# Kernel optimization log

Hardware: AMD Instinct MI355X
Metric: run time of the kernel (lower is better)

## Reference

```python
import jax, jax.numpy as jnp
import numpy as np

NH, HD = 8, 32  # num_heads, head_dim (fusion_dim=256)
BN_EPS = 1e-5

def conv1x1(x, W, b):
    # x: (B,Cin,H,W), W: (Cout,Cin), b: (Cout,)
    return jnp.einsum('oc,bchw->bohw', W, x) + b[None, :, None, None]

def mha(Q, K, V):
    # Q,K,V: (B,C,H,W); split channels into NH contiguous head chunks
    B, C, H, W = Q.shape
    N = H * W
    q = Q.reshape(B, NH, HD, N).transpose(0, 1, 3, 2)  # (B,nh,N,hd)
    k = K.reshape(B, NH, HD, N).transpose(0, 1, 3, 2)
    v = V.reshape(B, NH, HD, N).transpose(0, 1, 3, 2)
    scores = jnp.einsum('bhnd,bhmd->bhnm', q, k) / jnp.sqrt(jnp.float32(HD))
    attn = jax.nn.softmax(scores, axis=-1)  # dropout is identity in eval
    out = jnp.einsum('bhnm,bhmd->bhnd', attn, v)
    return out.transpose(0, 1, 3, 2).reshape(B, C, H, W)

def attention_map(Q, K, H, W):
    B, C = Q.shape[:2]
    N = H * W
    Qg = Q.reshape(B, NH, HD, N).mean(axis=-1)  # (B,nh,hd)
    Kg = K.reshape(B, NH, HD, N).mean(axis=-1)
    att = (Qg * Kg).sum(axis=-1).mean(axis=-1)  # (B,)
    return jnp.broadcast_to(att[:, None, None], (B, H, W))

def setup_inputs() -> dict:
    key = jax.random.key(0)
    ks = jax.random.split(key, 20)
    D = 256
    def w(k, o, i):
        return jax.random.normal(k, (o, i), dtype=jnp.float32) * 0.02
    def b(k, o):
        return jax.random.normal(k, (o,), dtype=jnp.float32) * 0.02
    return {
        'rgb_features': jax.random.normal(ks[0], (2, D, 56, 56), dtype=jnp.float32),
        'depth_features': jax.random.normal(ks[1], (2, D, 56, 56), dtype=jnp.float32),
        'Wq_rd': w(ks[2], D, D), 'bq_rd': b(ks[3], D),
        'Wk_d': w(ks[4], D, D), 'bk_d': b(ks[5], D),
        'Wv_d': w(ks[6], D, D), 'bv_d': b(ks[7], D),
        'Wq_dr': w(ks[8], D, D), 'bq_dr': b(ks[9], D),
        'Wk_r': w(ks[10], D, D), 'bk_r': b(ks[11], D),
        'Wv_r': w(ks[12], D, D), 'bv_r': b(ks[13], D),
        'Wf1': w(ks[14], D, 2 * D), 'bf1': b(ks[15], D),
        'gamma': jnp.ones((D,), jnp.float32), 'beta': jnp.zeros((D,), jnp.float32),
        'Wf2': w(ks[16], D, D), 'bf2': b(ks[17], D),
    }

def reference(rgb_features, depth_features, Wq_rd, bq_rd, Wk_d, bk_d, Wv_d, bv_d,
              Wq_dr, bq_dr, Wk_r, bk_r, Wv_r, bv_r, Wf1, bf1, gamma, beta, Wf2, bf2):
    B, _, H, W = rgb_features.shape
    Q_rgb = conv1x1(rgb_features, Wq_rd, bq_rd)
    K_depth = conv1x1(depth_features, Wk_d, bk_d)
    V_depth = conv1x1(depth_features, Wv_d, bv_d)
    rgb_attended = mha(Q_rgb, K_depth, V_depth)
    Q_depth = conv1x1(depth_features, Wq_dr, bq_dr)
    K_rgb = conv1x1(rgb_features, Wk_r, bk_r)
    V_rgb = conv1x1(rgb_features, Wv_r, bv_r)
    depth_attended = mha(Q_depth, K_rgb, V_rgb)
    fused = jnp.concatenate([rgb_attended, depth_attended], axis=1)
    h = conv1x1(fused, Wf1, bf1)
    # BatchNorm2d in eval mode: running_mean=0, running_var=1
    h = h / jnp.sqrt(jnp.float32(1.0 + BN_EPS)) * gamma[None, :, None, None] + beta[None, :, None, None]
    h = jax.nn.relu(h)
    fused_features = conv1x1(h, Wf2, bf2)
    amap = attention_map(Q_rgb, K_depth, H, W)
    return fused_features, amap
```

## Files before the change

### kernel.cpp

```cpp
#include <hip/hip_runtime.h>

typedef unsigned short u16;
typedef short bf8 __attribute__((ext_vector_type(8)));
typedef float f4 __attribute__((ext_vector_type(4)));
typedef unsigned short us4 __attribute__((ext_vector_type(4)));

#define DEV static __device__ __forceinline__

DEV u16 f2bf(float x) {
  union { float f; unsigned u; } v; v.f = x;
  unsigned r = v.u + 0x7fffu + ((v.u >> 16) & 1u);
  return (u16)(r >> 16);
}
DEV float bf2f(u16 h) {
  union { unsigned u; float f; } v; v.u = ((unsigned)h) << 16;
  return v.f;
}

constexpr int  NSP = 3136;
constexpr long SZ1 = 2l * 256 * NSP;
constexpr float SCQ = 0.2550205145980166f;
constexpr long OFF_XB  = 0;
constexpr long OFF_QB  = 2 * SZ1;
constexpr long OFF_KB  = 4 * SZ1;
constexpr long OFF_VB  = 6 * SZ1;
constexpr long OFF_ATT = 8 * SZ1;
constexpr long OFF_H   = 10 * SZ1;
constexpr long OFF_WC  = 11 * SZ1;
constexpr long OFF_WF1 = OFF_WC + 2l * 768 * 256;
constexpr long OFF_WF2 = OFF_WF1 + 256l * 512;
constexpr long END_BF16 = OFF_WF2 + 256l * 256;

__global__ __launch_bounds__(256) void k_cvt_x(const float* __restrict__ rgb,
                                               const float* __restrict__ dep,
                                               u16* __restrict__ xb) {
  __shared__ u16 xs[256][68];
  const int z = blockIdx.y;
  const int mod = z >> 1, b = z & 1;
  const float* s = (mod ? dep : rgb) + (long)b * 256 * NSP;
  const int n0 = blockIdx.x * 64;
  const int tid = threadIdx.x;
#pragma unroll
  for (int p = 0; p < 8; ++p) {
    const int c = p * 32 + (tid >> 3);
    const int nl = (tid & 7) * 8;
    f4 v0 = *(const f4*)(s + (long)c * NSP + n0 + nl);
    f4 v1 = *(const f4*)(s + (long)c * NSP + n0 + nl + 4);
    us4 o0, o1;
    o0.x = f2bf(v0.x); o0.y = f2bf(v0.y); o0.z = f2bf(v0.z); o0.w = f2bf(v0.w);
    o1.x = f2bf(v1.x); o1.y = f2bf(v1.y); o1.z = f2bf(v1.z); o1.w = f2bf(v1.w);
    *(us4*)(&xs[c][nl]) = o0;
    *(us4*)(&xs[c][nl + 4]) = o1;
  }
  __syncthreads();
  const int lane = tid & 63, ul = tid >> 6;
  const int g = lane >> 4, r = lane & 15;
  u16* dst = xb + (long)mod * SZ1 + (long)b * 802816
           + (((long)((n0 >> 4) + ul)) * 8) * 512 + lane * 8;
  const int nn = ul * 16 + r;
#pragma unroll
  for (int kblk = 0; kblk < 8; ++kblk) {
    const int c0 = kblk * 32 + g * 8;
    us4 lo, hi;
    lo.x = xs[c0 + 0][nn]; lo.y = xs[c0 + 1][nn]; lo.z = xs[c0 + 2][nn]; lo.w = xs[c0 + 3][nn];
    hi.x = xs[c0 + 4][nn]; hi.y = xs[c0 + 5][nn]; hi.z = xs[c0 + 6][nn]; hi.w = xs[c0 + 7][nn];
    *(us4*)(dst + kblk * 512) = lo;
    *(us4*)(dst + kblk * 512 + 4) = hi;
  }
}

__global__ __launch_bounds__(256) void k_prep(
    const float* __restrict__ wq_rd, const float* __restrict__ wk_r, const float* __restrict__ wv_r,
    const float* __restrict__ wq_dr, const float* __restrict__ wk_d, const float* __restrict__ wv_d,
    const float* __restrict__ wf1, const float* __restrict__ wf2,
    const float* __restrict__ bq_rd, const float* __restrict__ bk_r, const float* __restrict__ bv_r,
    const float* __restrict__ bq_dr, const float* __restrict__ bk_d, const float* __restrict__ bv_d,
    u16* __restrict__ wsb, float* __restrict__ bcat) {
  long idx = (long)blockIdx.x * 256 + threadIdx.x;
  const long WCN = 2l * 768 * 256;
  if (idx < WCN) {
    int mod = idx >= 768l * 256;
    long f = idx - (mod ? 768l * 256 : 0);
    int j = (int)f & 7, ln = ((int)f >> 3) & 63, unit = (int)(f >> 9);
    int kblk = unit & 7, mblk = unit >> 3;
    int row = mblk * 16 + (ln & 15), col = kblk * 32 + (ln >> 4) * 8 + j;
    int seg = row >> 8, r2 = row & 255;
    const float* src;
    if (!mod) src = seg == 0 ? wq_rd : (seg == 1 ? wk_r : wv_r);
    else      src = seg == 0 ? wq_dr : (seg == 1 ? wk_d : wv_d);
    wsb[OFF_WC + idx] = f2bf(src[r2 * 256 + col]);
    return;
  }
  long jx = idx - WCN;
  if (jx < 256l * 512) {
    int j = (int)jx & 7, ln = ((int)jx >> 3) & 63, unit = (int)(jx >> 9);
    int kblk = unit & 15, mblk = unit >> 4;
    int row = mblk * 16 + (ln & 15), col = kblk * 32 + (ln >> 4) * 8 + j;
    wsb[OFF_WF1 + jx] = f2bf(wf1[row * 512 + col]);
    return;
  }
  jx -= 256l * 512;
  if (jx < 256l * 256) {
    int j = (int)jx & 7, ln = ((int)jx >> 3) & 63, unit = (int)(jx >> 9);
    int kblk = unit & 7, mblk = unit >> 3;
    int row = mblk * 16 + (ln & 15), col = kblk * 32 + (ln >> 4) * 8 + j;
    wsb[OFF_WF2 + jx] = f2bf(wf2[row * 256 + col]);
    return;
  }
  jx -= 256l * 256;
  if (jx < 1536) {
    int mod = jx >= 768;
    int row = (int)jx - (mod ? 768 : 0);
    int seg = row >> 8, r2 = row & 255;
    const float* src;
    if (!mod) src = seg == 0 ? bq_rd : (seg == 1 ? bk_r : bv_r);
    else      src = seg == 0 ? bq_dr : (seg == 1 ? bk_d : bv_d);
    bcat[jx] = src[r2];
  }
}

template <int KDIM, int EPI>
__global__ __launch_bounds__(256) void k_gemm(
    u16* __restrict__ wsb, const float* __restrict__ bcat,
    const float* __restrict__ bf1, const float* __restrict__ gamma,
    const float* __restrict__ beta, const float* __restrict__ bf2,
    float* __restrict__ outf) {
  constexpr int KB = KDIM / 32;
  const int tid = threadIdx.x;
  const int lane = tid & 63, wid = tid >> 6;
  const int g = lane >> 4, r = lane & 15;
  const int wm = wid >> 1, wn = wid & 1;
  const int n0 = blockIdx.x * 64;
  const int m0 = blockIdx.y * 128;
  const int z = blockIdx.z;

  int b = 0, mod = 0;
  const u16* In; const u16* W;
  if constexpr (EPI == 0) {
    mod = z & 1; b = z >> 1;
    In = wsb + OFF_XB + (long)mod * SZ1 + (long)b * 802816;
    W  = wsb + OFF_WC + (long)mod * 768 * 256;
  } else if constexpr (EPI == 1) {
    b = z;
    In = wsb + OFF_ATT + (long)b * NSP * 512;
    W  = wsb + OFF_WF1;
  } else {
    b = z;
    In = wsb + OFF_H + (long)b * 802816;
    W  = wsb + OFF_WF2;
  }

  const int M0 = m0 + wm * 64;
  const u16* Abase = W + ((long)(M0 >> 4) * KB) * 512 + lane * 8;
  const u16* Bbase = In + ((long)((n0 >> 4) + wn * 2) * KB) * 512 + lane * 8;

  const f4 zero4 = {0.f, 0.f, 0.f, 0.f};
  f4 acc[4][2];
#pragma unroll
  for (int i = 0; i < 4; ++i)
#pragma unroll
    for (int j = 0; j < 2; ++j) acc[i][j] = zero4;

#pragma unroll 8
  for (int kb = 0; kb < KB; ++kb) {
    bf8 aw[4], bx[2];
#pragma unroll
    for (int i = 0; i < 4; ++i)
      aw[i] = *(const bf8*)(Abase + ((long)i * KB + kb) * 512);
#pragma unroll
    for (int jn = 0; jn < 2; ++jn)
      bx[jn] = *(const bf8*)(Bbase + ((long)jn * KB + kb) * 512);
#pragma unroll
    for (int i = 0; i < 4; ++i)
#pragma unroll
      for (int jn = 0; jn < 2; ++jn)
        acc[i][jn] = __builtin_amdgcn_mfma_f32_16x16x32_bf16(aw[i], bx[jn], acc[i][jn], 0, 0, 0);
  }

  const int seg = M0 >> 8;
#pragma unroll
  for (int i = 0; i < 4; ++i) {
    const int orow = M0 + i * 16 + 4 * g;
#pragma unroll
    for (int jn = 0; jn < 2; ++jn) {
      const int n = n0 + wn * 32 + jn * 16 + r;
      f4 a = acc[i][jn];
      if constexpr (EPI == 0) {
        const int ol = orow & 255;
        const float* bs = bcat + mod * 768 + seg * 256 + ol;
        const float qs = (seg == 0) ? SCQ : 1.0f;
        float a0 = (a.x + bs[0]) * qs, a1 = (a.y + bs[1]) * qs;
        float a2 = (a.z + bs[2]) * qs, a3 = (a.w + bs[3]) * qs;
        if (seg == 0) {
          const int hh = ol >> 5, hd0 = ol & 31;
          us4 pk; pk.x = f2bf(a0); pk.y = f2bf(a1); pk.z = f2bf(a2); pk.w = f2bf(a3);
          *(us4*)(wsb + OFF_QB + mod * SZ1
                  + (((long)(b * 8 + hh) * 196 + (n >> 4)) << 9)
                  + ((hd0 >> 3) * 16 + (n & 15)) * 8 + (hd0 & 7)) = pk;
        } else if (seg == 1) {
          const int hh = ol >> 5, hd0 = ol & 31;
          const int t = n >> 5, rr = n & 31;
          const int half = (rr >> 2) & 1, rK = ((rr >> 3) << 2) | (rr & 3);
          us4 pk; pk.x = f2bf(a0); pk.y = f2bf(a1); pk.z = f2bf(a2); pk.w = f2bf(a3);
          *(us4*)(wsb + OFF_KB + mod * SZ1
                  + ((((long)(b * 8 + hh) * 98 + t) * 2 + half) << 9)
                  + ((hd0 >> 3) * 16 + rK) * 8 + (hd0 & 7)) = pk;
        } else {
          const int hh = ol >> 5, rem = ol & 31, halfc = rem >> 4, rv = rem & 15;
          const int t = n >> 5, gp = (n >> 3) & 3, j = n & 7;
          u16* dst = wsb + OFF_VB + mod * SZ1
                   + ((((long)(b * 8 + hh) * 98 + t) * 2 + halfc) << 9)
                   + (gp * 16 + rv) * 8 + j;
          dst[0] = f2bf(a0); dst[8] = f2bf(a1); dst[16] = f2bf(a2); dst[24] = f2bf(a3);
        }
      } else if constexpr (EPI == 1) {
        us4 pk;
#pragma unroll
        for (int q = 0; q < 4; ++q) {
          const int o = orow + q;
          float v = (a[q] + bf1[o]) * (gamma[o] * 0.9999950000374994f) + beta[o];
          pk[q] = f2bf(fmaxf(v, 0.f));
        }
        const int ch0 = orow;
        *(us4*)(wsb + OFF_H + ((((long)b * 196 + (n >> 4)) * 8 + (ch0 >> 5)) << 9)
                + (((ch0 >> 3) & 3) * 16 + (n & 15)) * 8 + (ch0 & 7)) = pk;
      } else {
#pragma unroll
        for (int q = 0; q < 4; ++q) {
          const int o = orow + q;
          outf[(long)(b * 256 + o) * NSP + n] = a[q] + bf2[o];
        }
      }
    }
  }
}

DEV bf8 pack_p(f4 s0, f4 s1) {
  union { unsigned u[4]; bf8 v; } p;
  float a0 = __builtin_amdgcn_exp2f(s0.x), a1 = __builtin_amdgcn_exp2f(s0.y);
  float a2 = __builtin_amdgcn_exp2f(s0.z), a3 = __builtin_amdgcn_exp2f(s0.w);
  float a4 = __builtin_amdgcn_exp2f(s1.x), a5 = __builtin_amdgcn_exp2f(s1.y);
  float a6 = __builtin_amdgcn_exp2f(s1.z), a7 = __builtin_amdgcn_exp2f(s1.w);
  asm("v_cvt_pk_bf16_f32 %0, %1, %2" : "=v"(p.u[0]) : "v"(a0), "v"(a1));
  asm("v_cvt_pk_bf16_f32 %0, %1, %2" : "=v"(p.u[1]) : "v"(a2), "v"(a3));
  asm("v_cvt_pk_bf16_f32 %0, %1, %2" : "=v"(p.u[2]) : "v"(a4), "v"(a5));
  asm("v_cvt_pk_bf16_f32 %0, %1, %2" : "=v"(p.u[3]) : "v"(a6), "v"(a7));
  return p.v;
}

__global__ __launch_bounds__(256) void k_attn(u16* __restrict__ wsb) {
  const int m = blockIdx.z;
  const int bh = blockIdx.y;
  const int b = bh >> 3, h = bh & 7;
  const int tid = threadIdx.x;
  const int lane = tid & 63, wid = tid >> 6;
  const int qh = wid & 1, kvh = wid >> 1;
  const int g = lane >> 4, r = lane & 15;
  const int q0 = blockIdx.x * 64 + qh * 32;

  const u16* QF = wsb + OFF_QB + (long)m * SZ1 + ((long)bh * 196) * 512;
  const u16* KF = wsb + OFF_KB + (long)(1 - m) * SZ1 + ((long)bh * 196) * 512;
  const u16* VF = wsb + OFF_VB + (long)(1 - m) * SZ1 + ((long)bh * 196) * 512;

  const bf8 qfA = *(const bf8*)(QF + ((long)(q0 >> 4) << 9) + lane * 8);
  const bf8 qfB = *(const bf8*)(QF + ((long)((q0 >> 4) + 1) << 9) + lane * 8);
  const int kv0 = kvh ? 1600 : 0;
  const int kvn = kvh ? 1536 : 1600;
  const u16* kp = KF + ((long)(kv0 >> 5) << 10) + lane * 8;
  const u16* vp = VF + ((long)(kv0 >> 5) << 10) + lane * 8;

  bf8 ones;
#pragma unroll
  for (int j = 0; j < 8; ++j) ones[j] = (short)0x3F80;

  const f4 zero4 = {0.f, 0.f, 0.f, 0.f};
  f4 oA0 = zero4, oA1 = zero4, oB0 = zero4, oB1 = zero4;
  f4 lA = zero4, lB = zero4;

  for (int kv = 0; kv < kvn; kv += 64) {
    const bf8 kf0 = *(const bf8*)(kp);
    const bf8 kf1 = *(const bf8*)(kp + 512);
    const bf8 kf2 = *(const bf8*)(kp + 1024);
    const bf8 kf3 = *(const bf8*)(kp + 1536);
    kp += 2048;
    const bf8 v0a = *(const bf8*)(vp);
    const bf8 v1a = *(const bf8*)(vp + 512);
    const bf8 v0b = *(const bf8*)(vp + 1024);
    const bf8 v1b = *(const bf8*)(vp + 1536);
    vp += 2048;

    {
      f4 s0 = __builtin_amdgcn_mfma_f32_16x16x32_bf16(kf0, qfA, zero4, 0, 0, 0);
      f4 s1 = __builtin_amdgcn_mfma_f32_16x16x32_bf16(kf1, qfA, zero4, 0, 0, 0);
      f4 s2 = __builtin_amdgcn_mfma_f32_16x16x32_bf16(kf2, qfA, zero4, 0, 0, 0);
      f4 s3 = __builtin_amdgcn_mfma_f32_16x16x32_bf16(kf3, qfA, zero4, 0, 0, 0);
      bf8 p0 = pack_p(s0, s1);
      bf8 p1 = pack_p(s2, s3);
      lA  = __builtin_amdgcn_mfma_f32_16x16x32_bf16(ones, p0, lA, 0, 0, 0);
      lA  = __builtin_amdgcn_mfma_f32_16x16x32_bf16(ones, p1, lA, 0, 0, 0);
      oA0 = __builtin_amdgcn_mfma_f32_16x16x32_bf16(v0a, p0, oA0, 0, 0, 0);
      oA0 = __builtin_amdgcn_mfma_f32_16x16x32_bf16(v0b, p1, oA0, 0, 0, 0);
      oA1 = __builtin_amdgcn_mfma_f32_16x16x32_bf16(v1a, p0, oA1, 0, 0, 0);
      oA1 = __builtin_amdgcn_mfma_f32_16x16x32_bf16(v1b, p1, oA1, 0, 0, 0);
    }
    {
      f4 s0 = __builtin_amdgcn_mfma_f32_16x16x32_bf16(kf0, qfB, zero4, 0, 0, 0);
      f4 s1 = __builtin_amdgcn_mfma_f32_16x16x32_bf16(kf1, qfB, zero4, 0, 0, 0);
      f4 s2 = __builtin_amdgcn_mfma_f32_16x16x32_bf16(kf2, qfB, zero4, 0, 0, 0);
      f4 s3 = __builtin_amdgcn_mfma_f32_16x16x32_bf16(kf3, qfB, zero4, 0, 0, 0);
      bf8 p0 = pack_p(s0, s1);
      bf8 p1 = pack_p(s2, s3);
      lB  = __builtin_amdgcn_mfma_f32_16x16x32_bf16(ones, p0, lB, 0, 0, 0);
      lB  = __builtin_amdgcn_mfma_f32_16x16x32_bf16(ones, p1, lB, 0, 0, 0);
      oB0 = __builtin_amdgcn_mfma_f32_16x16x32_bf16(v0a, p0, oB0, 0, 0, 0);
      oB0 = __builtin_amdgcn_mfma_f32_16x16x32_bf16(v0b, p1, oB0, 0, 0, 0);
      oB1 = __builtin_amdgcn_mfma_f32_16x16x32_bf16(v1a, p0, oB1, 0, 0, 0);
      oB1 = __builtin_amdgcn_mfma_f32_16x16x32_bf16(v1b, p1, oB1, 0, 0, 0);
    }
  }

  __shared__ f4 so[2][4][64];
  __shared__ float sl[2][2][64];
  if (kvh) {
    so[qh][0][lane] = oA0; so[qh][1][lane] = oA1;
    so[qh][2][lane] = oB0; so[qh][3][lane] = oB1;
    sl[qh][0][lane] = lA.x; sl[qh][1][lane] = lB.x;
  }
  __syncthreads();
  if (!kvh) {
    oA0 += so[qh][0][lane]; oA1 += so[qh][1][lane];
    oB0 += so[qh][2][lane]; oB1 += so[qh][3][lane];
    const float invA = 1.0f / (lA.x + sl[qh][0][lane]);
    const float invB = 1.0f / (lB.x + sl[qh][1][lane]);
    oA0 *= invA; oA1 *= invA; oB0 *= invB; oB1 *= invB;

    u16* ab = wsb + OFF_ATT + ((((long)b * 196 + (q0 >> 4)) * 16) + m * 8 + h) * 512;
    const int ld0 = ((g >> 1) * 16 + r) * 8 + 4 * (g & 1);
    us4 w0, w1, w2, w3;
#pragma unroll
    for (int q = 0; q < 4; ++q) {
      w0[q] = f2bf(oA0[q]); w1[q] = f2bf(oA1[q]);
      w2[q] = f2bf(oB0[q]); w3[q] = f2bf(oB1[q]);
    }
    *(us4*)(ab + ld0) = w0;
    *(us4*)(ab + ld0 + 256) = w1;
    *(us4*)(ab + 8192 + ld0) = w2;
    *(us4*)(ab + 8192 + ld0 + 256) = w3;
  }
}

__global__ __launch_bounds__(256) void k_amap_red(const u16* __restrict__ wsb,
                                                  float* __restrict__ qsums,
                                                  float* __restrict__ ksums) {
  const int split = blockIdx.x;
  const int bh = blockIdx.y;
  const int t = threadIdx.x;
  const int d = t & 31, ns = t >> 5;
  const u16* qb = wsb + OFF_QB + ((long)bh * 196) * 512 + ((d >> 3) * 16) * 8 + (d & 7);
  const u16* kb = wsb + OFF_KB + SZ1 + ((long)bh * 196) * 512 + ((d >> 3) * 16) * 8 + (d & 7);
  float qs = 0.f, ks = 0.f;
  for (int u = split * 28 + ns; u < split * 28 + 28; u += 8) {
    const long ub = (long)u << 9;
#pragma unroll
    for (int rr = 0; rr < 16; ++rr) {
      qs += bf2f(qb[ub + rr * 8]);
      ks += bf2f(kb[ub + rr * 8]);
    }
  }
  __shared__ float sq[256], sk[256];
  sq[t] = qs; sk[t] = ks;
  __syncthreads();
  if (t < 32) {
#pragma unroll
    for (int j = 1; j < 8; ++j) { qs += sq[t + 32 * j]; ks += sk[t + 32 * j]; }
    atomicAdd(qsums + bh * 32 + t, qs);
    atomicAdd(ksums + bh * 32 + t, ks);
  }
}

__global__ __launch_bounds__(256) void k_amap_fin(const float* __restrict__ qsums,
                                                  const float* __restrict__ ksums,
                                                  float* __restrict__ att2) {
  const int b = blockIdx.x, t = threadIdx.x;
  float v = qsums[b * 256 + t] * ksums[b * 256 + t];
  __shared__ float sd[256];
  sd[t] = v; __syncthreads();
#pragma unroll
  for (int off = 128; off; off >>= 1) {
    if (t < off) sd[t] += sd[t + off];
    __syncthreads();
  }
  if (t == 0) att2[b] = sd[0] * (1.0f / (8.0f * 3136.0f * 3136.0f * SCQ));
}

__global__ void k_amap_wr(const float* __restrict__ att2, float* __restrict__ outf) {
  const int b = blockIdx.y;
  const int i = blockIdx.x * 256 + threadIdx.x;
  if (i < NSP) outf[2l * 256 * NSP + (long)b * NSP + i] = att2[b];
}

extern "C" void kernel_launch(void* const* d_in, const int* in_sizes, int n_in,
                              void* d_out, int out_size, void* d_ws, size_t ws_size,
                              hipStream_t stream) {
  const float* rgb   = (const float*)d_in[0];
  const float* dep   = (const float*)d_in[1];
  const float* Wq_rd = (const float*)d_in[2];
  const float* bq_rd = (const float*)d_in[3];
  const float* Wk_d  = (const float*)d_in[4];
  const float* bk_d  = (const float*)d_in[5];
  const float* Wv_d  = (const float*)d_in[6];
  const float* bv_d  = (const float*)d_in[7];
  const float* Wq_dr = (const float*)d_in[8];
  const float* bq_dr = (const float*)d_in[9];
  const float* Wk_r  = (const float*)d_in[10];
  const float* bk_r  = (const float*)d_in[11];
  const float* Wv_r  = (const float*)d_in[12];
  const float* bv_r  = (const float*)d_in[13];
  const float* Wf1   = (const float*)d_in[14];
  const float* bf1   = (const float*)d_in[15];
  const float* gamma = (const float*)d_in[16];
  const float* beta  = (const float*)d_in[17];
  const float* Wf2   = (const float*)d_in[18];
  const float* bf2   = (const float*)d_in[19];
  float* out = (float*)d_out;

  u16* wsb = (u16*)d_ws;
  float* wsf = (float*)((char*)d_ws + (size_t)END_BF16 * 2);
  float* att2  = wsf;
  float* qsums = wsf + 4;
  float* ksums = wsf + 4 + 512;
  float* bcat  = wsf + 4 + 1024;
  const size_t needed = (size_t)END_BF16 * 2 + (4 + 1024 + 1536) * sizeof(float);
  if (ws_size < needed) return;

  hipMemsetAsync(wsf, 0, (4 + 1024) * sizeof(float), stream);
  k_cvt_x<<<dim3(49, 4), 256, 0, stream>>>(rgb, dep, wsb);
  k_prep<<<2310, 256, 0, stream>>>(Wq_rd, Wk_r, Wv_r, Wq_dr, Wk_d, Wv_d, Wf1, Wf2,
                                   bq_rd, bk_r, bv_r, bq_dr, bk_d, bv_d, wsb, bcat);
  k_gemm<256, 0><<<dim3(49, 6, 4), 256, 0, stream>>>(wsb, bcat, nullptr, nullptr, nullptr, nullptr, nullptr);
  k_attn<<<dim3(49, 16, 2), 256, 0, stream>>>(wsb);
  k_amap_red<<<dim3(7, 16), 256, 0, stream>>>(wsb, qsums, ksums);
  k_amap_fin<<<2, 256, 0, stream>>>(qsums, ksums, att2);
  k_amap_wr<<<dim3(13, 2), 256, 0, stream>>>(att2, out);
  k_gemm<512, 1><<<dim3(49, 2, 2), 256, 0, stream>>>(wsb, nullptr, bf1, gamma, beta, nullptr, nullptr);
  k_gemm<256, 2><<<dim3(49, 2, 2), 256, 0, stream>>>(wsb, nullptr, nullptr, nullptr, nullptr, bf2, out);
}
```

Before: 119.0 us.

## Give each attention wave all 64 queries and split keys four ways

Each wave now processes all 64 query rows of the block (four Q fragments) against a quarter of the key/value range, instead of two waves per query half each taking half of the keys. Every K/V fragment loaded from global memory is therefore reused across four query tiles rather than two, halving K/V load traffic per unit of MFMA work. The cost is more accumulator registers per wave (8 output f4s plus 4 row sums), a larger shared-memory reduction across three waves, and a longer serial epilogue in wave 0.

Result: no change. 119.8 us (+0.7%).

```diff
diff --git a/kernel.cpp b/kernel.cpp
--- a/kernel.cpp
+++ b/kernel.cpp
@@ -253,31 +253,34 @@
   const int bh = blockIdx.y;
   const int b = bh >> 3, h = bh & 7;
   const int tid = threadIdx.x;
-  const int lane = tid & 63, wid = tid >> 6;
-  const int qh = wid & 1, kvh = wid >> 1;
+  const int lane = tid & 63, kvh = tid >> 6;
   const int g = lane >> 4, r = lane & 15;
-  const int q0 = blockIdx.x * 64 + qh * 32;
+  const int q0 = blockIdx.x * 64;
 
   const u16* QF = wsb + OFF_QB + (long)m * SZ1 + ((long)bh * 196) * 512;
   const u16* KF = wsb + OFF_KB + (long)(1 - m) * SZ1 + ((long)bh * 196) * 512;
   const u16* VF = wsb + OFF_VB + (long)(1 - m) * SZ1 + ((long)bh * 196) * 512;
 
-  const bf8 qfA = *(const bf8*)(QF + ((long)(q0 >> 4) << 9) + lane * 8);
-  const bf8 qfB = *(const bf8*)(QF + ((long)((q0 >> 4) + 1) << 9) + lane * 8);
-  const int kv0 = kvh ? 1600 : 0;
-  const int kvn = kvh ? 1536 : 1600;
-  const u16* kp = KF + ((long)(kv0 >> 5) << 10) + lane * 8;
-  const u16* vp = VF + ((long)(kv0 >> 5) << 10) + lane * 8;
+  bf8 qf[4];
+#pragma unroll
+  for (int j = 0; j < 4; ++j)
+    qf[j] = *(const bf8*)(QF + ((long)((q0 >> 4) + j) << 9) + lane * 8);
+
+  const int tb = kvh ? (13 + 12 * (kvh - 1)) : 0;
+  const int te = tb + (kvh ? 12 : 13);
+  const u16* kp = KF + ((long)tb << 11) + lane * 8;
+  const u16* vp = VF + ((long)tb << 11) + lane * 8;
 
   bf8 ones;
 #pragma unroll
   for (int j = 0; j < 8; ++j) ones[j] = (short)0x3F80;
 
   const f4 zero4 = {0.f, 0.f, 0.f, 0.f};
-  f4 oA0 = zero4, oA1 = zero4, oB0 = zero4, oB1 = zero4;
-  f4 lA = zero4, lB = zero4;
-
-  for (int kv = 0; kv < kvn; kv += 64) {
+  f4 o[4][2], l[4];
+#pragma unroll
+  for (int j = 0; j < 4; ++j) { o[j][0] = zero4; o[j][1] = zero4; l[j] = zero4; }
+
+  for (int t = tb; t < te; ++t) {
     const bf8 kf0 = *(const bf8*)(kp);
     const bf8 kf1 = *(const bf8*)(kp + 512);
     const bf8 kf2 = *(const bf8*)(kp + 1024);
@@ -289,63 +292,71 @@
     const bf8 v1b = *(const bf8*)(vp + 1536);
     vp += 2048;
 
-    {
-      f4 s0 = __builtin_amdgcn_mfma_f32_16x16x32_bf16(kf0, qfA, zero4, 0, 0, 0);
-      f4 s1 = __builtin_amdgcn_mfma_f32_16x16x32_bf16(kf1, qfA, zero4, 0, 0, 0);
-      f4 s2 = __builtin_amdgcn_mfma_f32_16x16x32_bf16(kf2, qfA, zero4, 0, 0, 0);
-      f4 s3 = __builtin_amdgcn_mfma_f32_16x16x32_bf16(kf3, qfA, zero4, 0, 0, 0);
-      bf8 p0 = pack_p(s0, s1);
-      bf8 p1 = pack_p(s2, s3);
-      lA  = __builtin_amdgcn_mfma_f32_16x16x32_bf16(ones, p0, lA, 0, 0, 0);
-      lA  = __builtin_amdgcn_mfma_f32_16x16x32_bf16(ones, p1, lA, 0, 0, 0);
-      oA0 = __builtin_amdgcn_mfma_f32_16x16x32_bf16(v0a, p0, oA0, 0, 0, 0);
-      oA0 = __builtin_amdgcn_mfma_f32_16x16x32_bf16(v0b, p1, oA0, 0, 0, 0);
-      oA1 = __builtin_amdgcn_mfma_f32_16x16x32_bf16(v1a, p0, oA1, 0, 0, 0);
-      oA1 = __builtin_amdgcn_mfma_f32_16x16x32_bf16(v1b, p1, oA1, 0, 0, 0);
+#pragma unroll
+    for (int pr = 0; pr < 2; ++pr) {
+      const bf8 qA = qf[pr * 2], qB = qf[pr * 2 + 1];
+      f4 sA0 = __builtin_amdgcn_mfma_f32_16x16x32_bf16(kf0, qA, zero4, 0, 0, 0);
+      f4 sA1 = __builtin_amdgcn_mfma_f32_16x16x32_bf16(kf1, qA, zero4, 0, 0, 0);
+      f4 sA2 = __builtin_amdgcn_mfma_f32_16x16x32_bf16(kf2, qA, zero4, 0, 0, 0);
+      f4 sA3 = __builtin_amdgcn_mfma_f32_16x16x32_bf16(kf3, qA, zero4, 0, 0, 0);
+      f4 sB0 = __builtin_amdgcn_mfma_f32_16x16x32_bf16(kf0, qB, zero4, 0, 0, 0);
+      f4 sB1 = __builtin_amdgcn_mfma_f32_16x16x32_bf16(kf1, qB, zero4, 0, 0, 0);
+      f4 sB2 = __builtin_amdgcn_mfma_f32_16x16x32_bf16(kf2, qB, zero4, 0, 0, 0);
+      f4 sB3 = __builtin_amdgcn_mfma_f32_16x16x32_bf16(kf3, qB, zero4, 0, 0, 0);
+      bf8 pA0 = pack_p(sA0, sA1);
+      bf8 pA1 = pack_p(sA2, sA3);
+      bf8 pB0 = pack_p(sB0, sB1);
+      bf8 pB1 = pack_p(sB2, sB3);
+      const int jA = pr * 2, jB = pr * 2 + 1;
+      l[jA]    = __builtin_amdgcn_mfma_f32_16x16x32_bf16(ones, pA0, l[jA], 0, 0, 0);
+      l[jA]    = __builtin_amdgcn_mfma_f32_16x16x32_bf16(ones, pA1, l[jA], 0, 0, 0);
+      l[jB]    = __builtin_amdgcn_mfma_f32_16x16x32_bf16(ones, pB0, l[jB], 0, 0, 0);
+      l[jB]    = __builtin_amdgcn_mfma_f32_16x16x32_bf16(ones, pB1, l[jB], 0, 0, 0);
+      o[jA][0] = __builtin_amdgcn_mfma_f32_16x16x32_bf16(v0a, pA0, o[jA][0], 0, 0, 0);
+      o[jA][0] = __builtin_amdgcn_mfma_f32_16x16x32_bf16(v0b, pA1, o[jA][0], 0, 0, 0);
+      o[jA][1] = __builtin_amdgcn_mfma_f32_16x16x32_bf16(v1a, pA0, o[jA][1], 0, 0, 0);
+      o[jA][1] = __builtin_amdgcn_mfma_f32_16x16x32_bf16(v1b, pA1, o[jA][1], 0, 0, 0);
+      o[jB][0] = __builtin_amdgcn_mfma_f32_16x16x32_bf16(v0a, pB0, o[jB][0], 0, 0, 0);
+      o[jB][0] = __builtin_amdgcn_mfma_f32_16x16x32_bf16(v0b, pB1, o[jB][0], 0, 0, 0);
+      o[jB][1] = __builtin_amdgcn_mfma_f32_16x16x32_bf16(v1a, pB0, o[jB][1], 0, 0, 0);
+      o[jB][1] = __builtin_amdgcn_mfma_f32_16x16x32_bf16(v1b, pB1, o[jB][1], 0, 0, 0);
     }
-    {
-      f4 s0 = __builtin_amdgcn_mfma_f32_16x16x32_bf16(kf0, qfB, zero4, 0, 0, 0);
-      f4 s1 = __builtin_amdgcn_mfma_f32_16x16x32_bf16(kf1, qfB, zero4, 0, 0, 0);
-      f4 s2 = __builtin_amdgcn_mfma_f32_16x16x32_bf16(kf2, qfB, zero4, 0, 0, 0);
-      f4 s3 = __builtin_amdgcn_mfma_f32_16x16x32_bf16(kf3, qfB, zero4, 0, 0, 0);
-      bf8 p0 = pack_p(s0, s1);
-      bf8 p1 = pack_p(s2, s3);
-      lB  = __builtin_amdgcn_mfma_f32_16x16x32_bf16(ones, p0, lB, 0, 0, 0);
-      lB  = __builtin_amdgcn_mfma_f32_16x16x32_bf16(ones, p1, lB, 0, 0, 0);
-      oB0 = __builtin_amdgcn_mfma_f32_16x16x32_bf16(v0a, p0, oB0, 0, 0, 0);
-      oB0 = __builtin_amdgcn_mfma_f32_16x16x32_bf16(v0b, p1, oB0, 0, 0, 0);
-      oB1 = __builtin_amdgcn_mfma_f32_16x16x32_bf16(v1a, p0, oB1, 0, 0, 0);
-      oB1 = __builtin_amdgcn_mfma_f32_16x16x32_bf16(v1b, p1, oB1, 0, 0, 0);
+  }
+
+  __shared__ f4 so[3][8][64];
+  __shared__ float sl[3][4][64];
+  if (kvh) {
+#pragma unroll
+    for (int j = 0; j < 4; ++j) {
+      so[kvh - 1][j * 2][lane] = o[j][0];
+      so[kvh - 1][j * 2 + 1][lane] = o[j][1];
+      sl[kvh - 1][j][lane] = l[j].x;
     }
-  }
-
-  __shared__ f4 so[2][4][64];
-  __shared__ float sl[2][2][64];
-  if (kvh) {
-    so[qh][0][lane] = oA0; so[qh][1][lane] = oA1;
-    so[qh][2][lane] = oB0; so[qh][3][lane] = oB1;
-    sl[qh][0][lane] = lA.x; sl[qh][1][lane] = lB.x;
   }
   __syncthreads();
   if (!kvh) {
-    oA0 += so[qh][0][lane]; oA1 += so[qh][1][lane];
-    oB0 += so[qh][2][lane]; oB1 += so[qh][3][lane];
-    const float invA = 1.0f / (lA.x + sl[qh][0][lane]);
-    const float invB = 1.0f / (lB.x + sl[qh][1][lane]);
-    oA0 *= invA; oA1 *= invA; oB0 *= invB; oB1 *= invB;
-
+#pragma unroll
+    for (int w = 0; w < 3; ++w)
+#pragma unroll
+      for (int j = 0; j < 4; ++j) {
+        o[j][0] += so[w][j * 2][lane];
+        o[j][1] += so[w][j * 2 + 1][lane];
+        l[j].x += sl[w][j][lane];
+      }
     u16* ab = wsb + OFF_ATT + ((((long)b * 196 + (q0 >> 4)) * 16) + m * 8 + h) * 512;
     const int ld0 = ((g >> 1) * 16 + r) * 8 + 4 * (g & 1);
-    us4 w0, w1, w2, w3;
-#pragma unroll
-    for (int q = 0; q < 4; ++q) {
-      w0[q] = f2bf(oA0[q]); w1[q] = f2bf(oA1[q]);
-      w2[q] = f2bf(oB0[q]); w3[q] = f2bf(oB1[q]);
+#pragma unroll
+    for (int j = 0; j < 4; ++j) {
+      const float inv = 1.0f / l[j].x;
+      us4 w0, w1;
+#pragma unroll
+      for (int q = 0; q < 4; ++q) {
+        w0[q] = f2bf(o[j][0][q] * inv);
+        w1[q] = f2bf(o[j][1][q] * inv);
+      }
+      *(us4*)(ab + j * 8192 + ld0) = w0;
+      *(us4*)(ab + j * 8192 + ld0 + 256) = w1;
     }
-    *(us4*)(ab + ld0) = w0;
-    *(us4*)(ab + ld0 + 256) = w1;
-    *(us4*)(ab + 8192 + ld0) = w2;
-    *(us4*)(ab + 8192 + ld0 + 256) = w3;
   }
 }
 
```
